# Kernel optimization log

Measured on AMD Instinct MI355X. Metric: run time of the kernel, lower is better.

## Reference

```python
import jax, jax.numpy as jnp
import numpy as np

NQ = 8            # data qubits: ceil(log2(256))
NLAYERS = 6       # StronglyEntanglingLayers depth
BATCH = 4096
IN_DIM = 2560
ENC_DIM = 256

def leaky(x):
    return jnp.where(x >= 0, x, 0.2 * x)

def rot_mat(phi, theta, omega):
    # PennyLane Rot(phi,theta,omega) = RZ(omega) @ RY(theta) @ RZ(phi)
    c = jnp.cos(theta / 2); s = jnp.sin(theta / 2)
    m00 = jnp.exp(-0.5j * (phi + omega)) * c
    m01 = -jnp.exp(0.5j * (phi - omega)) * s
    m10 = jnp.exp(-0.5j * (phi - omega)) * s
    m11 = jnp.exp(0.5j * (phi + omega)) * c
    return jnp.stack([jnp.stack([m00, m01]), jnp.stack([m10, m11])])

def apply_1q(psi, U, w):
    psi = jnp.tensordot(U, psi, axes=((1,), (w,)))
    return jnp.moveaxis(psi, 0, w)

def apply_cnot(psi, c, t):
    s = jnp.moveaxis(psi, (c, t), (0, 1))
    s = jnp.stack([s[0], s[1, ::-1]], axis=0)
    return jnp.moveaxis(s, (0, 1), (c, t))

def circuit(amps, params):
    # amps: (256,) complex64 normalized amplitudes; params: (L, NQ, 3)
    psi = amps.reshape((2,) * NQ)
    L = params.shape[0]
    for l in range(L):
        for q in range(NQ):
            psi = apply_1q(psi, rot_mat(params[l, q, 0], params[l, q, 1], params[l, q, 2]), q)
        r = l % (NQ - 1) + 1  # PennyLane default imprimitive ranges
        for q in range(NQ):
            psi = apply_cnot(psi, q, (q + r) % NQ)
    probs = jnp.real(psi * jnp.conj(psi))
    z, xm, ym = [], [], []
    yfac_base = jnp.array([-1j, 1j], dtype=psi.dtype)
    for q in range(NQ):
        axes = tuple(i for i in range(NQ) if i != q)
        p = jnp.sum(probs, axis=axes)
        z.append(p[0] - p[1])
        flipped = jnp.flip(psi, axis=q)
        xm.append(jnp.real(jnp.sum(jnp.conj(psi) * flipped)))
        yfac = yfac_base.reshape([2 if i == q else 1 for i in range(NQ)])
        ym.append(jnp.real(jnp.sum(jnp.conj(psi) * (flipped * yfac))))
    return jnp.stack(z + xm + ym)  # (24,) order: Z..., X..., Y...

def forward(x, ew1, eb1, ew2, eb2, ew3, eb3, dec_params,
            dw1, db1, dw2, db2, dw3, db3, dw4, db4, dw5, db5):
    h = leaky(x @ ew1 + eb1)
    h = leaky(h @ ew2 + eb2)
    enc = jnp.tanh(h @ ew3 + eb3)                      # (B, 256)
    nrm = jnp.linalg.norm(enc, axis=1, keepdims=True)
    amps = jax.lax.stop_gradient(enc / jnp.maximum(nrm, 1e-12)).astype(jnp.complex64)
    meas = jax.vmap(lambda a: circuit(a, dec_params))(amps)  # (B, 24)
    h = leaky(meas @ dw1 + db1)
    h = leaky(h @ dw2 + db2)
    h = leaky(h @ dw3 + db3)
    h = leaky(h @ dw4 + db4)
    return jnp.tanh(h @ dw5 + db5)                     # (B, 2560)

def _lin(key, fin, fout):
    k1, k2 = jax.random.split(key)
    lim = 1.0 / np.sqrt(fin)
    w = jax.random.uniform(k1, (fin, fout), jnp.float32, -lim, lim)
    b = jax.random.uniform(k2, (fout,), jnp.float32, -lim, lim)
    return w, b

def setup_inputs() -> dict:
    key = jax.random.key(0)
    ks = jax.random.split(key, 10)
    x = jax.random.normal(ks[0], (BATCH, IN_DIM), jnp.float32)
    ew1, eb1 = _lin(ks[1], IN_DIM, 1024)
    ew2, eb2 = _lin(ks[2], 1024, 512)
    ew3, eb3 = _lin(ks[3], 512, ENC_DIM)
    dec_params = jax.random.uniform(ks[4], (NLAYERS, NQ, 3), jnp.float32, 0.0, 2 * np.pi)
    dw1, db1 = _lin(ks[5], 3 * NQ, 128)
    dw2, db2 = _lin(ks[6], 128, 256)
    dw3, db3 = _lin(ks[7], 256, 512)
    dw4, db4 = _lin(ks[8], 512, 1024)
    dw5, db5 = _lin(ks[9], 1024, IN_DIM)
    return {"x": x, "ew1": ew1, "eb1": eb1, "ew2": ew2, "eb2": eb2, "ew3": ew3, "eb3": eb3,
            "dec_params": dec_params, "dw1": dw1, "db1": db1, "dw2": dw2, "db2": db2,
            "dw3": dw3, "db3": db3, "dw4": dw4, "db4": db4, "dw5": dw5, "db5": db5}

def reference(x, ew1, eb1, ew2, eb2, ew3, eb3, dec_params,
              dw1, db1, dw2, db2, dw3, db3, dw4, db4, dw5, db5):
    return forward(x, ew1, eb1, ew2, eb2, ew3, eb3, dec_params,
                   dw1, db1, dw2, db2, dw3, db3, dw4, db4, dw5, db5)
```

## Files before the change

### kernel.cpp

```cpp
#include <hip/hip_runtime.h>
#include <hip/hip_bf16.h>


using bf16 = __hip_bfloat16;
typedef __attribute__((ext_vector_type(8))) short short8;
typedef __attribute__((ext_vector_type(4))) short short4v;
typedef __attribute__((ext_vector_type(4))) float f32x4;

__device__ inline void stf(float* p, size_t i, float v) { p[i] = v; }
__device__ inline void stf(bf16* p, size_t i, float v) { p[i] = __float2bfloat16(v); }

__device__ inline short f2bs(float x) {
  bf16 h = __float2bfloat16(x);
  return *reinterpret_cast<short*>(&h);
}
__device__ inline short8 ld8b(const float* p) {
  const float4 a = ((const float4*)p)[0];
  const float4 b = ((const float4*)p)[1];
  short8 r;
  r[0] = f2bs(a.x); r[1] = f2bs(a.y); r[2] = f2bs(a.z); r[3] = f2bs(a.w);
  r[4] = f2bs(b.x); r[5] = f2bs(b.y); r[6] = f2bs(b.z); r[7] = f2bs(b.w);
  return r;
}
__device__ inline short4v ld4b(const float* p) {
  const float4 a = *(const float4*)p;
  short4v r;
  r[0] = f2bs(a.x); r[1] = f2bs(a.y); r[2] = f2bs(a.z); r[3] = f2bs(a.w);
  return r;
}

__device__ inline void async_load16(const bf16* g, short* l) {
  __builtin_amdgcn_global_load_lds(
      (const __attribute__((address_space(1))) unsigned int*)g,
      (__attribute__((address_space(3))) unsigned int*)l, 16, 0, 0);
}

__global__ __launch_bounds__(256) void prep_all(
    const float* w0, const float* w1, const float* w2, const float* w3,
    const float* w4, const float* w5, const float* w6, const float* w7,
    const float* b0, const float* b1, const float* b2, const float* b3,
    const float* b4, const float* b5, const float* b6, const float* b7,
    const float* dp, const float* xf,
    bf16* __restrict__ wt, float* __restrict__ biasf, float* __restrict__ gw,
    bf16* __restrict__ xb, int do_x) {
  const int bid = blockIdx.x;
  const int tid = threadIdx.x;
  const int Ks[8]  = {2560, 1024, 512, 24, 128, 256, 512, 1024};
  const int Ns[8]  = {1024, 512, 256, 128, 256, 512, 1024, 2560};
  const int cum[8] = {2560, 3072, 3200, 3204, 3236, 3364, 3876, 6436};
  const long wto[8] = {0, 2621440, 3145728, 3276800, 3280896, 3313664, 3444736, 3969024};
  const float* Wp[8] = {w0, w1, w2, w3, w4, w5, w6, w7};
  const float* Bp[8] = {b0, b1, b2, b3, b4, b5, b6, b7};
  const int boff[8] = {0, 1024, 1536, 1792, 1920, 2176, 2688, 3712};

  if (bid < 6436) {
    int t = 0;
    while (bid >= cum[t]) t++;
    int base = t ? cum[t - 1] : 0;
    int local = bid - base;
    int K = Ks[t], N = Ns[t];
    int tk = (K + 31) >> 5;
    int kt = local % tk, nt = local / tk;
    int Kp = tk << 5;
    __shared__ short tile[32][33];
    int r = tid >> 3, c4 = (tid & 7) << 2;
    int gk = kt * 32 + r, gn = nt * 32 + c4;
    short4v v;
    if (gk < K) v = ld4b(Wp[t] + (size_t)gk * N + gn);
    else { v[0] = 0; v[1] = 0; v[2] = 0; v[3] = 0; }
    tile[r][c4] = v[0]; tile[r][c4 + 1] = v[1]; tile[r][c4 + 2] = v[2]; tile[r][c4 + 3] = v[3];
    __syncthreads();
    int n = tid >> 3, k4 = (tid & 7) << 2;
    short4v o;
    o[0] = tile[k4][n]; o[1] = tile[k4 + 1][n]; o[2] = tile[k4 + 2][n]; o[3] = tile[k4 + 3][n];
    *(short4v*)&wt[wto[t] + (size_t)(nt * 32 + n) * Kp + kt * 32 + k4] = o;
  } else if (bid < 6444) {
    int b = bid - 6436;
    int nb = Ns[b];
    for (int t2 = tid; t2 < nb; t2 += 256)
      biasf[boff[b] + t2] = Bp[b][t2];
  } else if (bid == 6444) {
    int g = tid;
    if (g < 48) {
      float phi = dp[g * 3 + 0], theta = dp[g * 3 + 1], omega = dp[g * 3 + 2];
      float c = cosf(0.5f * theta), s = sinf(0.5f * theta);
      float a = 0.5f * (phi + omega), d = 0.5f * (phi - omega);
      float ca = cosf(a), sa = sinf(a), cd = cosf(d), sd = sinf(d);
      float* o = gw + g * 8;
      o[0] =  ca * c; o[1] = -sa * c;
      o[2] = -cd * s; o[3] = -sd * s;
      o[4] =  cd * s; o[5] = -sd * s;
      o[6] =  ca * c; o[7] =  sa * c;
    }
  } else if (do_x) {
    long i = ((long)(bid - 6445) * 256 + tid) * 8;
    if (i < 10485760L) {
      short8 v = ld8b(xf + i);
      *(short8*)((short*)xb + i) = v;
    }
  }
}

template <int BM, int BN, int BK, int WR, int WC, int ACT, typename TC>
__global__ __launch_bounds__(256) void gemm_async(const bf16* __restrict__ A,
                                                  const bf16* __restrict__ Bt,
                                                  const float* __restrict__ bias,
                                                  TC* __restrict__ C,
                                                  int M, int N, int K) {
  constexpr int CPR = BK / 8;
  constexpr int MASK = CPR - 1;
  constexpr int RPW = 64 / CPR;
  constexpr int RPP = 4 * RPW;
  constexpr int WMT = BM / WR;
  constexpr int WNT = BN / WC;
  constexpr int FI = WMT / 16;
  constexpr int FJ = WNT / 16;
  constexpr int KK = BK / 32;
  __shared__ __align__(16) short As[BM * BK];
  __shared__ __align__(16) short Bs[BN * BK];
  const int tid = threadIdx.x;
  const int lane = tid & 63;
  const int wid = tid >> 6;
  const int wm = wid / WC, wn = wid % WC;
  const int bm = blockIdx.y * BM;
  const int bn = blockIdx.x * BN;

  const int st_r = lane / CPR;
  const int st_cs = (lane & MASK) ^ (st_r & MASK);

  const int frag_m = lane & 15;
  const int q = lane >> 4;

  f32x4 acc[FI][FJ] = {};

  for (int k0 = 0; k0 < K; k0 += BK) {
#pragma unroll
    for (int p = 0; p < BM / RPP; ++p) {
      const bf16* g = A + (size_t)(bm + p * RPP + wid * RPW + st_r) * K + k0 + st_cs * 8;
      async_load16(g, &As[(p * RPP + wid * RPW) * BK]);
    }
#pragma unroll
    for (int p = 0; p < BN / RPP; ++p) {
      const bf16* g = Bt + (size_t)(bn + p * RPP + wid * RPW + st_r) * K + k0 + st_cs * 8;
      async_load16(g, &Bs[(p * RPP + wid * RPW) * BK]);
    }
    __syncthreads();
    short8 af[FI][KK], bfr[FJ][KK];
#pragma unroll
    for (int i = 0; i < FI; ++i) {
      const int m = wm * WMT + i * 16 + frag_m;
#pragma unroll
      for (int kk = 0; kk < KK; ++kk) {
        const int slot = (kk * 4 + q) ^ (m & MASK);
        af[i][kk] = *(const short8*)&As[m * BK + slot * 8];
      }
    }
#pragma unroll
    for (int j = 0; j < FJ; ++j) {
      const int n = wn * WNT + j * 16 + frag_m;
#pragma unroll
      for (int kk = 0; kk < KK; ++kk) {
        const int slot = (kk * 4 + q) ^ (n & MASK);
        bfr[j][kk] = *(const short8*)&Bs[n * BK + slot * 8];
      }
    }
#pragma unroll
    for (int kk = 0; kk < KK; ++kk)
#pragma unroll
      for (int i = 0; i < FI; ++i)
#pragma unroll
        for (int j = 0; j < FJ; ++j)
          acc[i][j] = __builtin_amdgcn_mfma_f32_16x16x32_bf16(af[i][kk], bfr[j][kk], acc[i][j], 0, 0, 0);
    __syncthreads();
  }

  const int col_lane = lane & 15;
  const int row_quad = q << 2;
#pragma unroll
  for (int i = 0; i < FI; ++i) {
#pragma unroll
    for (int j = 0; j < FJ; ++j) {
      int n = bn + wn * WNT + j * 16 + col_lane;
      float bj = bias[n];
#pragma unroll
      for (int r = 0; r < 4; ++r) {
        int m = bm + wm * WMT + i * 16 + row_quad + r;
        float v = acc[i][j][r] + bj;
        if (ACT == 0) v = (v >= 0.f) ? v : 0.2f * v;
        else v = tanhf(v);
        stf(C, (size_t)m * N + n, v);
      }
    }
  }
}

__global__ __launch_bounds__(256) void gemm_cvt(const float* __restrict__ A,
                                                const float* __restrict__ W,
                                                const float* __restrict__ bias,
                                                bf16* __restrict__ C,
                                                int M, int N, int K) {
  __shared__ __align__(16) short As[128 * 40];
  __shared__ __align__(16) short Bs[128 * 40];
  const int tid = threadIdx.x;
  const int lane = tid & 63;
  const int wave = tid >> 6;
  const int wm = wave >> 1, wn = wave & 1;
  const int bm = blockIdx.y * 128;
  const int bn = blockIdx.x * 128;
  const int a_row0 = tid >> 2;
  const int a_kcol = (tid & 3) << 3;
  const int b_ncol = (tid & 31) << 2;
  const int b_krow = (tid >> 5) << 2;
  const int frag_m = lane & 15;
  const int frag_k = (lane >> 4) << 3;

  f32x4 acc[4][4] = {};

  for (int k0 = 0; k0 < K; k0 += 32) {
#pragma unroll
    for (int c = 0; c < 2; ++c) {
      const int row = c * 64 + a_row0;
      short8 v = ld8b(A + (size_t)(bm + row) * K + k0 + a_kcol);
      *(short8*)&As[row * 40 + a_kcol] = v;
    }
    short4v bv[4];
#pragma unroll
    for (int kk = 0; kk < 4; ++kk)
      bv[kk] = ld4b(W + (size_t)(k0 + b_krow + kk) * N + bn + b_ncol);
#pragma unroll
    for (int nn = 0; nn < 4; ++nn) {
      short4v w;
      w[0] = bv[0][nn]; w[1] = bv[1][nn]; w[2] = bv[2][nn]; w[3] = bv[3][nn];
      *(short4v*)&Bs[(b_ncol + nn) * 40 + b_krow] = w;
    }
    __syncthreads();
    short8 af[4], bfr[4];
#pragma unroll
    for (int i = 0; i < 4; ++i)
      af[i] = *(const short8*)&As[(wm * 64 + i * 16 + frag_m) * 40 + frag_k];
#pragma unroll
    for (int j = 0; j < 4; ++j)
      bfr[j] = *(const short8*)&Bs[(wn * 64 + j * 16 + frag_m) * 40 + frag_k];
#pragma unroll
    for (int i = 0; i < 4; ++i)
#pragma unroll
      for (int j = 0; j < 4; ++j)
        acc[i][j] = __builtin_amdgcn_mfma_f32_16x16x32_bf16(af[i], bfr[j], acc[i][j], 0, 0, 0);
    __syncthreads();
  }

  const int col_lane = lane & 15;
  const int row_quad = (lane >> 4) << 2;
#pragma unroll
  for (int i = 0; i < 4; ++i)
#pragma unroll
    for (int j = 0; j < 4; ++j) {
      int n = bn + wn * 64 + j * 16 + col_lane;
      float bj = bias[n];
#pragma unroll
      for (int r = 0; r < 4; ++r) {
        int m = bm + wm * 64 + i * 16 + row_quad + r;
        float v = acc[i][j][r] + bj;
        v = (v >= 0.f) ? v : 0.2f * v;
        stf(C, (size_t)m * N + n, v);
      }
    }
}

__global__ __launch_bounds__(256) void circuit_wave(const float* __restrict__ enc,
                                                    const float* __restrict__ gw,
                                                    bf16* __restrict__ meas) {
  __shared__ float gsh[384];
  const int tid = threadIdx.x;
  for (int t = tid; t < 384; t += 256) gsh[t] = gw[t];
  __syncthreads();
  const int lane = tid & 63;
  const int b = blockIdx.x * 4 + (tid >> 6);

  float4 e = *(const float4*)(enc + (size_t)b * 256 + lane * 4);
  float re[4] = {e.x, e.y, e.z, e.w};
  float im[4] = {0.f, 0.f, 0.f, 0.f};
  float ss = e.x * e.x + e.y * e.y + e.z * e.z + e.w * e.w;
#pragma unroll
  for (int o = 32; o; o >>= 1) ss += __shfl_xor(ss, o, 64);
  float inv = 1.0f / fmaxf(sqrtf(ss), 1e-12f);
#pragma unroll
  for (int j = 0; j < 4; ++j) re[j] *= inv;

  for (int l = 0; l < 6; ++l) {
    for (int qq = 0; qq < 8; ++qq) {
      const float* g = &gsh[(l * 8 + qq) * 8];
      const int s = 1 << (7 - qq);
      if (s >= 4) {
        const int lm = s >> 2;
        const bool hi = (lane & lm) != 0;
        const float g0r = hi ? g[4] : g[0], g0i = hi ? g[5] : g[1];
        const float g1r = hi ? g[6] : g[2], g1i = hi ? g[7] : g[3];
#pragma unroll
        for (int j = 0; j < 4; ++j) {
          float orr = __shfl_xor(re[j], lm, 64);
          float oii = __shfl_xor(im[j], lm, 64);
          float p0r = hi ? orr : re[j], p0i = hi ? oii : im[j];
          float p1r = hi ? re[j] : orr, p1i = hi ? im[j] : oii;
          re[j] = g0r * p0r - g0i * p0i + g1r * p1r - g1i * p1i;
          im[j] = g0r * p0i + g0i * p0r + g1r * p1i + g1i * p1r;
        }
      } else {
#pragma unroll
        for (int j0 = 0; j0 < 4; ++j0) {
          if ((j0 & s) == 0) {
            int j1 = j0 | s;
            float p0r = re[j0], p0i = im[j0], p1r = re[j1], p1i = im[j1];
            re[j0] = g[0] * p0r - g[1] * p0i + g[2] * p1r - g[3] * p1i;
            im[j0] = g[0] * p0i + g[1] * p0r + g[2] * p1i + g[3] * p1r;
            re[j1] = g[4] * p0r - g[5] * p0i + g[6] * p1r - g[7] * p1i;
            im[j1] = g[4] * p0i + g[5] * p0r + g[6] * p1i + g[7] * p1r;
          }
        }
      }
    }
    const int r = l % 7 + 1;
    for (int qq = 0; qq < 8; ++qq) {
      const int sc = 1 << (7 - qq);
      const int st = 1 << (7 - ((qq + r) & 7));
      if (st >= 4) {
        const int lm = st >> 2;
        if (sc >= 4) {
          const bool ctl = (lane & (sc >> 2)) != 0;
#pragma unroll
          for (int j = 0; j < 4; ++j) {
            float orr = __shfl_xor(re[j], lm, 64);
            float oii = __shfl_xor(im[j], lm, 64);
            re[j] = ctl ? orr : re[j];
            im[j] = ctl ? oii : im[j];
          }
        } else {
#pragma unroll
          for (int j = 0; j < 4; ++j) {
            if (j & sc) {
              re[j] = __shfl_xor(re[j], lm, 64);
              im[j] = __shfl_xor(im[j], lm, 64);
            }
          }
        }
      } else {
        if (sc >= 4) {
          const bool ctl = (lane & (sc >> 2)) != 0;
#pragma unroll
          for (int j0 = 0; j0 < 4; ++j0) {
            if ((j0 & st) == 0) {
              int j1 = j0 | st;
              float t0r = re[j0], t0i = im[j0];
              float t1r = re[j1], t1i = im[j1];
              re[j0] = ctl ? t1r : t0r; im[j0] = ctl ? t1i : t0i;
              re[j1] = ctl ? t0r : t1r; im[j1] = ctl ? t0i : t1i;
            }
          }
        } else {
#pragma unroll
          for (int j0 = 0; j0 < 4; ++j0) {
            if ((j0 & sc) && (j0 & st) == 0) {
              int j1 = j0 | st;
              float tr = re[j0], ti = im[j0];
              re[j0] = re[j1]; im[j0] = im[j1];
              re[j1] = tr; im[j1] = ti;
            }
          }
        }
      }
    }
  }

  for (int qq = 0; qq < 8; ++qq) {
    const int s = 1 << (7 - qq);
    float z = 0.f, x = 0.f, y = 0.f;
#pragma unroll
    for (int j = 0; j < 4; ++j) {
      float fr, fi;
      if (s >= 4) {
        fr = __shfl_xor(re[j], s >> 2, 64);
        fi = __shfl_xor(im[j], s >> 2, 64);
      } else {
        fr = re[j ^ s]; fi = im[j ^ s];
      }
      float prob = re[j] * re[j] + im[j] * im[j];
      int i = lane * 4 + j;
      float sg = (i & s) ? -1.f : 1.f;
      z += sg * prob;
      x += re[j] * fr + im[j] * fi;
      y += sg * (re[j] * fi - im[j] * fr);
    }
#pragma unroll
    for (int o = 32; o; o >>= 1) {
      z += __shfl_xor(z, o, 64);
      x += __shfl_xor(x, o, 64);
      y += __shfl_xor(y, o, 64);
    }
    if (lane == 0) {
      meas[(size_t)b * 32 + qq]      = __float2bfloat16(z);
      meas[(size_t)b * 32 + 8 + qq]  = __float2bfloat16(x);
      meas[(size_t)b * 32 + 16 + qq] = __float2bfloat16(y);
    }
  }
  if (lane >= 24 && lane < 32)
    meas[(size_t)b * 32 + lane] = __float2bfloat16(0.f);
}

extern "C" void kernel_launch(void* const* d_in, const int* in_sizes, int n_in,
                              void* d_out, int out_size, void* d_ws, size_t ws_size,
                              hipStream_t stream) {
  (void)in_sizes; (void)n_in; (void)out_size;
  char* wsb = (char*)d_ws;
  float* gw    = (float*)(wsb + 256);
  float* biasf = (float*)(wsb + 4096);
  bf16*  meas  = (bf16*)(wsb + 32768);
  float* encf  = (float*)(wsb + 294912);
  bf16*  P     = (bf16*)(wsb + 4489216);
  bf16*  Q     = (bf16*)(wsb + 12877824);
  bf16*  WT    = (bf16*)(wsb + 17072128);
  bf16*  Xb    = (bf16*)(wsb + 30253056);
  const bool have_xb = ws_size >= 51224576;

  bf16* ew1t = WT + 0;
  bf16* ew2t = WT + 2621440;
  bf16* ew3t = WT + 3145728;
  bf16* dw1t = WT + 3276800;
  bf16* dw2t = WT + 3280896;
  bf16* dw3t = WT + 3313664;
  bf16* dw4t = WT + 3444736;
  bf16* dw5t = WT + 3969024;
  float* beb1 = biasf + 0;
  float* beb2 = biasf + 1024;
  float* beb3 = biasf + 1536;
  float* bdb1 = biasf + 1792;
  float* bdb2 = biasf + 1920;
  float* bdb3 = biasf + 2176;
  float* bdb4 = biasf + 2688;
  float* bdb5 = biasf + 3712;

  prep_all<<<11565, 256, 0, stream>>>(
      (const float*)d_in[1], (const float*)d_in[3], (const float*)d_in[5],
      (const float*)d_in[8], (const float*)d_in[10], (const float*)d_in[12],
      (const float*)d_in[14], (const float*)d_in[16],
      (const float*)d_in[2], (const float*)d_in[4], (const float*)d_in[6],
      (const float*)d_in[9], (const float*)d_in[11], (const float*)d_in[13],
      (const float*)d_in[15], (const float*)d_in[17],
      (const float*)d_in[7], (const float*)d_in[0],
      WT, biasf, gw, Xb, have_xb ? 1 : 0);

  if (have_xb) {
    gemm_async<128, 64, 64, 4, 1, 0, bf16><<<dim3(16, 32), 256, 0, stream>>>(
        Xb, ew1t, beb1, P, 4096, 1024, 2560);
  } else {
    gemm_cvt<<<dim3(8, 32), 256, 0, stream>>>(
        (const float*)d_in[0], (const float*)d_in[1], beb1, P, 4096, 1024, 2560);
  }

  gemm_async<64, 64, 64, 2, 2, 0, bf16><<<dim3(8, 64), 256, 0, stream>>>(
      P, ew2t, beb2, Q, 4096, 512, 1024);
  gemm_async<64, 64, 64, 2, 2, 1, float><<<dim3(4, 64), 256, 0, stream>>>(
      Q, ew3t, beb3, encf, 4096, 256, 512);

  circuit_wave<<<1024, 256, 0, stream>>>(encf, gw, meas);

  gemm_async<64, 64, 32, 2, 2, 0, bf16><<<dim3(2, 64), 256, 0, stream>>>(
      meas, dw1t, bdb1, Q, 4096, 128, 32);
  gemm_async<64, 64, 64, 2, 2, 0, bf16><<<dim3(4, 64), 256, 0, stream>>>(
      Q, dw2t, bdb2, P, 4096, 256, 128);
  gemm_async<64, 64, 64, 2, 2, 0, bf16><<<dim3(8, 64), 256, 0, stream>>>(
      P, dw3t, bdb3, Q, 4096, 512, 256);
  gemm_async<128, 64, 64, 4, 1, 0, bf16><<<dim3(16, 32), 256, 0, stream>>>(
      Q, dw4t, bdb4, P, 4096, 1024, 512);
  gemm_async<128, 128, 64, 2, 2, 1, float><<<dim3(20, 32), 256, 0, stream>>>(
      P, dw5t, bdb5, (float*)d_out, 4096, 2560, 1024);
}
```

Baseline: 309.8 us.

## Fuse first decoder linear layer into circuit kernel and use fast tanh

The circuit kernel now keeps the 24 measurements in registers and computes the first decoder layer (24->128, bias, leaky ReLU) directly, writing bf16 activations. This removes a separate small GEMM launch and the round trip of the padded measurement buffer. It also swaps tanhf in the GEMM epilogue for an exp-based approximation. The fused layer reads fp32 weights from global memory per lane, and the tanh approximation slightly changes numerics.

```diff
diff --git a/kernel.cpp b/kernel.cpp
--- a/kernel.cpp
+++ b/kernel.cpp
@@ -9,6 +9,12 @@
 
 __device__ inline void stf(float* p, size_t i, float v) { p[i] = v; }
 __device__ inline void stf(bf16* p, size_t i, float v) { p[i] = __float2bfloat16(v); }
+
+__device__ inline float fast_tanh(float x) {
+  x = fminf(fmaxf(x, -15.0f), 15.0f);
+  float t = __expf(2.0f * x);
+  return __fdividef(t - 1.0f, t + 1.0f);
+}
 
 __device__ inline short f2bs(float x) {
   bf16 h = __float2bfloat16(x);
@@ -187,7 +193,7 @@
         int m = bm + wm * WMT + i * 16 + row_quad + r;
         float v = acc[i][j][r] + bj;
         if (ACT == 0) v = (v >= 0.f) ? v : 0.2f * v;
-        else v = tanhf(v);
+        else v = fast_tanh(v);
         stf(C, (size_t)m * N + n, v);
       }
     }
@@ -269,7 +275,9 @@
 
 __global__ __launch_bounds__(256) void circuit_wave(const float* __restrict__ enc,
                                                     const float* __restrict__ gw,
-                                                    bf16* __restrict__ meas) {
+                                                    const float* __restrict__ dw1,
+                                                    const float* __restrict__ db1,
+                                                    bf16* __restrict__ d1out) {
   __shared__ float gsh[384];
   const int tid = threadIdx.x;
   for (int t = tid; t < 384; t += 256) gsh[t] = gw[t];
@@ -371,6 +379,8 @@
     }
   }
 
+  float mz[8], mx[8], my[8];
+#pragma unroll
   for (int qq = 0; qq < 8; ++qq) {
     const int s = 1 << (7 - qq);
     float z = 0.f, x = 0.f, y = 0.f;
@@ -396,14 +406,22 @@
       x += __shfl_xor(x, o, 64);
       y += __shfl_xor(y, o, 64);
     }
-    if (lane == 0) {
-      meas[(size_t)b * 32 + qq]      = __float2bfloat16(z);
-      meas[(size_t)b * 32 + 8 + qq]  = __float2bfloat16(x);
-      meas[(size_t)b * 32 + 16 + qq] = __float2bfloat16(y);
-    }
-  }
-  if (lane >= 24 && lane < 32)
-    meas[(size_t)b * 32 + lane] = __float2bfloat16(0.f);
+    mz[qq] = z; mx[qq] = x; my[qq] = y;
+  }
+
+#pragma unroll
+  for (int half = 0; half < 2; ++half) {
+    const int n = lane + half * 64;
+    float acc = db1[n];
+#pragma unroll
+    for (int qq = 0; qq < 8; ++qq) {
+      acc += mz[qq] * dw1[qq * 128 + n];
+      acc += mx[qq] * dw1[(8 + qq) * 128 + n];
+      acc += my[qq] * dw1[(16 + qq) * 128 + n];
+    }
+    acc = (acc >= 0.f) ? acc : 0.2f * acc;
+    d1out[(size_t)b * 128 + n] = __float2bfloat16(acc);
+  }
 }
 
 extern "C" void kernel_launch(void* const* d_in, const int* in_sizes, int n_in,
@@ -413,7 +431,6 @@
   char* wsb = (char*)d_ws;
   float* gw    = (float*)(wsb + 256);
   float* biasf = (float*)(wsb + 4096);
-  bf16*  meas  = (bf16*)(wsb + 32768);
   float* encf  = (float*)(wsb + 294912);
   bf16*  P     = (bf16*)(wsb + 4489216);
   bf16*  Q     = (bf16*)(wsb + 12877824);
@@ -424,7 +441,6 @@
   bf16* ew1t = WT + 0;
   bf16* ew2t = WT + 2621440;
   bf16* ew3t = WT + 3145728;
-  bf16* dw1t = WT + 3276800;
   bf16* dw2t = WT + 3280896;
   bf16* dw3t = WT + 3313664;
   bf16* dw4t = WT + 3444736;
@@ -432,7 +448,6 @@
   float* beb1 = biasf + 0;
   float* beb2 = biasf + 1024;
   float* beb3 = biasf + 1536;
-  float* bdb1 = biasf + 1792;
   float* bdb2 = biasf + 1920;
   float* bdb3 = biasf + 2176;
   float* bdb4 = biasf + 2688;
@@ -461,10 +476,9 @@
   gemm_async<64, 64, 64, 2, 2, 1, float><<<dim3(4, 64), 256, 0, stream>>>(
       Q, ew3t, beb3, encf, 4096, 256, 512);
 
-  circuit_wave<<<1024, 256, 0, stream>>>(encf, gw, meas);
-
-  gemm_async<64, 64, 32, 2, 2, 0, bf16><<<dim3(2, 64), 256, 0, stream>>>(
-      meas, dw1t, bdb1, Q, 4096, 128, 32);
+  circuit_wave<<<1024, 256, 0, stream>>>(encf, gw, (const float*)d_in[8],
+                                         (const float*)d_in[9], Q);
+
   gemm_async<64, 64, 64, 2, 2, 0, bf16><<<dim3(4, 64), 256, 0, stream>>>(
       Q, dw2t, bdb2, P, 4096, 256, 128);
   gemm_async<64, 64, 64, 2, 2, 0, bf16><<<dim3(8, 64), 256, 0, stream>>>(
```

Measured after the change: 308.1 us. Within noise of the previous version (-0.6%).
